# Optimization experiments

Measured on AMD Instinct MI355X. Metric: run time of the kernel, lower is better.

The kernel has to match this reference:

```python
import jax, jax.numpy as jnp
import numpy as np

B, T, C = 16, 2048, 1024
HEAD = 64

def setup_inputs() -> dict:
    key = jax.random.key(0)
    kx, kq, kk, kv = jax.random.split(key, 4)
    x = jax.random.normal(kx, (B, T, C), dtype=jnp.float32)
    s = 1.0 / np.sqrt(C)
    Wq = jax.random.normal(kq, (C, HEAD), dtype=jnp.float32) * s
    Wk = jax.random.normal(kk, (C, HEAD), dtype=jnp.float32) * s
    Wv = jax.random.normal(kv, (C, HEAD), dtype=jnp.float32) * s
    return {"x": x, "Wq": Wq, "Wk": Wk, "Wv": Wv}

def reference(x, Wq, Wk, Wv):
    Bb, Tt, Cc = x.shape
    q = jnp.einsum('btc,ch->bth', x, Wq)  # [B,T,H]
    k = jnp.einsum('btc,ch->bth', x, Wk)
    v = jnp.einsum('btc,ch->bth', x, Wv)
    # NOTE: source scales by C**-0.5 (n_embd), not head_size**-0.5
    scores = jnp.einsum('bth,bsh->bts', q, k) * (Cc ** -0.5)  # [B,T,T]
    causal = jnp.tril(jnp.ones((Tt, Tt), dtype=bool))
    scores = jnp.where(causal, scores, -jnp.inf)
    attn = jax.nn.softmax(scores, axis=-1)  # dropout p=0 -> identity
    out = jnp.einsum('bts,bsh->bth', attn, v)  # [B,T,H]
    return out
```

## Files before the change

### kernel.cpp

```cpp
#include <hip/hip_runtime.h>

typedef __bf16 bf16;
typedef __bf16 bf16x2 __attribute__((ext_vector_type(2)));
typedef __bf16 bf16x4 __attribute__((ext_vector_type(4)));
typedef __bf16 bf16x8 __attribute__((ext_vector_type(8)));
typedef float f32x4 __attribute__((ext_vector_type(4)));

#define TT_ 2048
#define CC_ 1024
#define HH_ 64

#define SCALE2 0.045084221f

static __device__ __forceinline__ unsigned pack_bf16(float a, float b) {
    union { bf16x2 h; unsigned u; } z;
    z.h = bf16x2{(bf16)a, (bf16)b};
    return z.u;
}
static __device__ __forceinline__ void plswap32(unsigned &a, unsigned &b) {
    asm("v_permlane32_swap_b32 %0, %1" : "+v"(a), "+v"(b));
}
static __device__ __forceinline__ void plswap16(unsigned &a, unsigned &b) {
    asm("v_permlane16_swap_b32 %0, %1" : "+v"(a), "+v"(b));
}

__global__ __launch_bounds__(256) void prep_w(const float* __restrict__ Wq,
                                              const float* __restrict__ Wk,
                                              const float* __restrict__ Wv,
                                              bf16* __restrict__ Wt) {
    __shared__ bf16 Ls[64 * 65];
    const int m  = blockIdx.x >> 4;
    const int k0 = (blockIdx.x & 15) * 64;
    const float* W = (m == 0) ? Wq : (m == 1) ? Wk : Wv;
    const int tid = threadIdx.x;
    #pragma unroll
    for (int j = 0; j < 4; ++j) {
        int idx = tid + 256 * j;
        int r   = idx >> 4;
        int c4  = (idx & 15) * 4;
        float4 w = *(const float4*)&W[(size_t)(k0 + r) * HH_ + c4];
        Ls[r * 65 + c4 + 0] = (bf16)w.x;
        Ls[r * 65 + c4 + 1] = (bf16)w.y;
        Ls[r * 65 + c4 + 2] = (bf16)w.z;
        Ls[r * 65 + c4 + 3] = (bf16)w.w;
    }
    __syncthreads();
    #pragma unroll
    for (int j = 0; j < 4; ++j) {
        int idx = tid + 256 * j;
        int n   = idx >> 4;
        int kc  = (idx & 15) * 4;
        bf16x4 v;
        #pragma unroll
        for (int i = 0; i < 4; ++i) v[i] = Ls[(kc + i) * 65 + n];
        *(bf16x4*)&Wt[m * 65536 + n * 1024 + k0 + kc] = v;
    }
}

__global__ __launch_bounds__(256, 3) void qkv_kernel(const float* __restrict__ x,
                                                     const bf16* __restrict__ Wt,
                                                     bf16* __restrict__ qb,
                                                     bf16* __restrict__ kb,
                                                     bf16* __restrict__ vt) {
    __shared__ __align__(16) bf16 Xs[64 * 72];
    const int tid  = threadIdx.x;
    const int wave = tid >> 6;
    const int lane = tid & 15;
    const int quad = (tid & 63) >> 4;
    const int m0   = blockIdx.x * 64;

    f32x4 acc[4][3];
    #pragma unroll
    for (int i = 0; i < 4; ++i)
        #pragma unroll
        for (int j = 0; j < 3; ++j) acc[i][j] = f32x4{0.f, 0.f, 0.f, 0.f};

    const float* xrow[4];
    #pragma unroll
    for (int rt = 0; rt < 4; ++rt)
        xrow[rt] = x + (size_t)(m0 + rt * 16 + lane) * CC_ + quad * 8;
    const bf16* wbase = Wt + (size_t)(wave * 48 + lane) * 1024 + quad * 8;

    for (int kbi = 0; kbi < 16; ++kbi) {
        const int k0 = kbi * 64;
        bf16x8 afr[2][4];
        #pragma unroll
        for (int step = 0; step < 2; ++step)
            #pragma unroll
            for (int rt = 0; rt < 4; ++rt) {
                float4 a = *(const float4*)&xrow[rt][k0 + step * 32];
                float4 b = *(const float4*)&xrow[rt][k0 + step * 32 + 4];
                afr[step][rt] = bf16x8{(bf16)a.x, (bf16)a.y, (bf16)a.z, (bf16)a.w,
                                       (bf16)b.x, (bf16)b.y, (bf16)b.z, (bf16)b.w};
            }
        bf16x8 bfr[2][3];
        #pragma unroll
        for (int step = 0; step < 2; ++step)
            #pragma unroll
            for (int ct = 0; ct < 3; ++ct)
                bfr[step][ct] = *(const bf16x8*)&wbase[(size_t)(ct * 16) * 1024 + k0 + step * 32];
        #pragma unroll
        for (int step = 0; step < 2; ++step)
            #pragma unroll
            for (int ct = 0; ct < 3; ++ct)
                #pragma unroll
                for (int rt = 0; rt < 4; ++rt)
                    acc[rt][ct] = __builtin_amdgcn_mfma_f32_16x16x32_bf16(afr[step][rt], bfr[step][ct], acc[rt][ct], 0, 0, 0);
    }

    const int bb = m0 >> 11;
    const int t0 = m0 & 2047;
    #pragma unroll
    for (int ct = 0; ct < 3; ++ct) {
        int c0 = wave * 48 + ct * 16;
        if (c0 < 64) {
            int h = c0 + lane;
            #pragma unroll
            for (int rt = 0; rt < 4; ++rt)
                #pragma unroll
                for (int r = 0; r < 4; ++r)
                    qb[(size_t)(m0 + rt * 16 + quad * 4 + r) * HH_ + h] = (bf16)(acc[rt][ct][r] * SCALE2);
        } else if (c0 < 128) {
            int h = (c0 - 64) + lane;
            #pragma unroll
            for (int rt = 0; rt < 4; ++rt)
                #pragma unroll
                for (int r = 0; r < 4; ++r)
                    kb[(size_t)(m0 + rt * 16 + quad * 4 + r) * HH_ + h] = (bf16)acc[rt][ct][r];
        } else {
            int h = (c0 - 128) + lane;
            #pragma unroll
            for (int rt = 0; rt < 4; ++rt)
                #pragma unroll
                for (int r = 0; r < 4; ++r)
                    Xs[(rt * 16 + quad * 4 + r) * 72 + h] = (bf16)acc[rt][ct][r];
        }
    }
    __syncthreads();
    {
        int h  = tid >> 2;
        int tc = (tid & 3) * 16;
        bf16x8 v0, v1;
        #pragma unroll
        for (int i = 0; i < 8; ++i) v0[i] = Xs[(tc + i) * 72 + h];
        #pragma unroll
        for (int i = 0; i < 8; ++i) v1[i] = Xs[(tc + 8 + i) * 72 + h];
        bf16* dst = &vt[(size_t)bb * HH_ * TT_ + (size_t)h * TT_ + t0 + tc];
        *(bf16x8*)dst = v0;
        *(bf16x8*)(dst + 8) = v1;
    }
}

__global__ __launch_bounds__(256, 2) void attn_kernel(const bf16* __restrict__ qb,
                                                      const bf16* __restrict__ kb,
                                                      const bf16* __restrict__ vt,
                                                      float* __restrict__ out) {
    __shared__ __align__(16) bf16 Ks[128 * 72];
    __shared__ __align__(16) bf16 Vs[64 * 136];

    const int tid  = threadIdx.x;
    const int wave = tid >> 6;
    const int lane = tid & 15;
    const int quad = (tid & 63) >> 4;

    const int j  = blockIdx.x;
    const int bb = j & 15;
    const int p  = j >> 4;
    const int qi = (p < 16) ? p : 47 - p;
    const int nch = (qi >> 1) + 1;

    const int qrow  = qi * 64 + wave * 16;
    const int qg    = qrow + lane;
    const int qmaxw = qrow + 15;

    const int krow = tid >> 3, kc8 = (tid & 7) * 8;
    const int vh   = tid >> 4, vc8 = (tid & 15) * 8;
    const bf16* kp = kb + (size_t)(bb * TT_ + krow) * HH_ + kc8;
    const bf16* vp = vt + (size_t)bb * HH_ * TT_ + (size_t)vh * TT_ + vc8;

    bf16x8 kr[4], vvr[4];
    #pragma unroll
    for (int j2 = 0; j2 < 4; ++j2) kr[j2]  = *(const bf16x8*)&kp[(size_t)j2 * 32 * HH_];
    #pragma unroll
    for (int j2 = 0; j2 < 4; ++j2) vvr[j2] = *(const bf16x8*)&vp[j2 * 16 * TT_];

    bf16x8 aq[2];
    #pragma unroll
    for (int step = 0; step < 2; ++step)
        aq[step] = *(const bf16x8*)&qb[(size_t)(bb * TT_ + qg) * HH_ + step * 32 + quad * 8];

    bf16x8 vones;
    #pragma unroll
    for (int i = 0; i < 8; ++i) vones[i] = (bf16)1.0f;

    f32x4 o_acc[4];
    #pragma unroll
    for (int ht = 0; ht < 4; ++ht) o_acc[ht] = f32x4{0.f, 0.f, 0.f, 0.f};
    f32x4 lacc = f32x4{0.f, 0.f, 0.f, 0.f};

    for (int c = 0; c < nch; ++c) {
        const int s0 = c * 128;
        __syncthreads();
        #pragma unroll
        for (int j2 = 0; j2 < 4; ++j2) *(bf16x8*)&Ks[(krow + 32 * j2) * 72 + kc8] = kr[j2];
        #pragma unroll
        for (int j2 = 0; j2 < 4; ++j2) *(bf16x8*)&Vs[(vh + 16 * j2) * 136 + vc8]  = vvr[j2];
        __syncthreads();
        if (c + 1 < nch) {
            #pragma unroll
            for (int j2 = 0; j2 < 4; ++j2)
                kr[j2] = *(const bf16x8*)&kp[(size_t)((c + 1) * 128 + j2 * 32) * HH_];
            #pragma unroll
            for (int j2 = 0; j2 < 4; ++j2)
                vvr[j2] = *(const bf16x8*)&vp[(c + 1) * 128 + j2 * 16 * TT_];
        }

        const bool msk = (c == nch - 1);
        #pragma unroll
        for (int w = 0; w < 4; ++w) {
            if (msk && (s0 + w * 32 > qmaxw)) continue;
            const bool haveB = !msk || (s0 + w * 32 + 16 <= qmaxw);

            f32x4 sA = {0.f, 0.f, 0.f, 0.f};
            f32x4 sB = {0.f, 0.f, 0.f, 0.f};
            __builtin_amdgcn_s_setprio(1);
            {
                bf16x8 ak0 = *(const bf16x8*)&Ks[(w * 32 + lane) * 72 + quad * 8];
                bf16x8 ak1 = *(const bf16x8*)&Ks[(w * 32 + lane) * 72 + 32 + quad * 8];
                sA = __builtin_amdgcn_mfma_f32_16x16x32_bf16(ak0, aq[0], sA, 0, 0, 0);
                sA = __builtin_amdgcn_mfma_f32_16x16x32_bf16(ak1, aq[1], sA, 0, 0, 0);
            }
            if (haveB) {
                bf16x8 bk0 = *(const bf16x8*)&Ks[(w * 32 + 16 + lane) * 72 + quad * 8];
                bf16x8 bk1 = *(const bf16x8*)&Ks[(w * 32 + 16 + lane) * 72 + 32 + quad * 8];
                sB = __builtin_amdgcn_mfma_f32_16x16x32_bf16(bk0, aq[0], sB, 0, 0, 0);
                sB = __builtin_amdgcn_mfma_f32_16x16x32_bf16(bk1, aq[1], sB, 0, 0, 0);
            }
            __builtin_amdgcn_s_setprio(0);

            const int kA0 = s0 + w * 32 + quad * 4;
            float eA[4], eB[4];
            #pragma unroll
            for (int r = 0; r < 4; ++r) {
                float e = __builtin_amdgcn_exp2f(sA[r]);
                if (msk && (kA0 + r > qg)) e = 0.f;
                eA[r] = e;
            }
            if (haveB) {
                #pragma unroll
                for (int r = 0; r < 4; ++r) {
                    float e = __builtin_amdgcn_exp2f(sB[r]);
                    if (msk && (kA0 + 16 + r > qg)) e = 0.f;
                    eB[r] = e;
                }
            } else {
                #pragma unroll
                for (int r = 0; r < 4; ++r) eB[r] = 0.f;
            }

            unsigned d0 = pack_bf16(eA[0], eA[1]);
            unsigned d1 = pack_bf16(eA[2], eA[3]);
            unsigned d2 = pack_bf16(eB[0], eB[1]);
            unsigned d3 = pack_bf16(eB[2], eB[3]);
            plswap32(d0, d2);
            plswap16(d0, d2);
            plswap32(d1, d3);
            plswap16(d1, d3);
            union { unsigned u[4]; bf16x8 v; } apu;
            apu.u[0] = d0; apu.u[1] = d1; apu.u[2] = d2; apu.u[3] = d3;

            __builtin_amdgcn_s_setprio(1);
            #pragma unroll
            for (int ht = 0; ht < 4; ++ht) {
                bf16x8 bv = *(const bf16x8*)&Vs[(ht * 16 + lane) * 136 + w * 32 + quad * 8];
                o_acc[ht] = __builtin_amdgcn_mfma_f32_16x16x32_bf16(apu.v, bv, o_acc[ht], 0, 0, 0);
            }
            lacc = __builtin_amdgcn_mfma_f32_16x16x32_bf16(apu.v, vones, lacc, 0, 0, 0);
            __builtin_amdgcn_s_setprio(0);
        }
    }

    float inv[4];
    #pragma unroll
    for (int r = 0; r < 4; ++r) inv[r] = __builtin_amdgcn_rcpf(lacc[r]);
    #pragma unroll
    for (int ht = 0; ht < 4; ++ht)
        #pragma unroll
        for (int r = 0; r < 4; ++r)
            out[(size_t)(bb * TT_ + qrow + quad * 4 + r) * HH_ + ht * 16 + lane] = o_acc[ht][r] * inv[r];
}

extern "C" void kernel_launch(void* const* d_in, const int* in_sizes, int n_in,
                              void* d_out, int out_size, void* d_ws, size_t ws_size,
                              hipStream_t stream) {
    const float* x  = (const float*)d_in[0];
    const float* Wq = (const float*)d_in[1];
    const float* Wk = (const float*)d_in[2];
    const float* Wv = (const float*)d_in[3];
    float* out = (float*)d_out;

    char* ws = (char*)d_ws;
    bf16*  qb = (bf16*)(ws);
    bf16*  kb = (bf16*)(ws + 4194304);
    bf16*  vt = (bf16*)(ws + 8388608);
    bf16*  Wt = (bf16*)(ws + 12582912);

    prep_w<<<48, 256, 0, stream>>>(Wq, Wk, Wv, Wt);
    qkv_kernel<<<512, 256, 0, stream>>>(x, Wt, qb, kb, vt);
    attn_kernel<<<512, 256, 0, stream>>>(qb, kb, vt, out);
}
```

Before: 289.2 us.

## Prefetch x tiles into per-wave LDS double buffer and halve QKV tile rows

New measurement: 293.1 us. Within noise of the previous version (+1.4%).

```diff
diff --git a/kernel.cpp b/kernel.cpp
--- a/kernel.cpp
+++ b/kernel.cpp
@@ -57,42 +57,53 @@
     }
 }
 
-__global__ __launch_bounds__(256, 3) void qkv_kernel(const float* __restrict__ x,
+__global__ __launch_bounds__(256, 4) void qkv_kernel(const float* __restrict__ x,
                                                      const bf16* __restrict__ Wt,
                                                      bf16* __restrict__ qb,
                                                      bf16* __restrict__ kb,
                                                      bf16* __restrict__ vt) {
-    __shared__ __align__(16) bf16 Xs[64 * 72];
+    __shared__ __align__(16) bf16 Xs[4][2][32 * 72];
     const int tid  = threadIdx.x;
     const int wave = tid >> 6;
+    const int wl   = tid & 63;
     const int lane = tid & 15;
     const int quad = (tid & 63) >> 4;
-    const int m0   = blockIdx.x * 64;
-
-    f32x4 acc[4][3];
-    #pragma unroll
-    for (int i = 0; i < 4; ++i)
+    const int m0   = blockIdx.x * 32;
+
+    bf16 (*myXs)[32 * 72] = Xs[wave];
+
+    const int srow = wl >> 1;
+    const int scol = (wl & 1) * 32;
+    const float* xsrc = x + (size_t)(m0 + srow) * CC_ + scol;
+    const bf16*  wbase = Wt + (size_t)(wave * 48 + lane) * 1024 + quad * 8;
+
+    f32x4 acc[2][3];
+    #pragma unroll
+    for (int i = 0; i < 2; ++i)
         #pragma unroll
         for (int j = 0; j < 3; ++j) acc[i][j] = f32x4{0.f, 0.f, 0.f, 0.f};
 
-    const float* xrow[4];
-    #pragma unroll
-    for (int rt = 0; rt < 4; ++rt)
-        xrow[rt] = x + (size_t)(m0 + rt * 16 + lane) * CC_ + quad * 8;
-    const bf16* wbase = Wt + (size_t)(wave * 48 + lane) * 1024 + quad * 8;
+    float4 pf[8];
+    #pragma unroll
+    for (int i = 0; i < 8; ++i) pf[i] = *(const float4*)&xsrc[i * 4];
+    #pragma unroll
+    for (int i = 0; i < 4; ++i) {
+        bf16x8 bv = {(bf16)pf[2*i].x, (bf16)pf[2*i].y, (bf16)pf[2*i].z, (bf16)pf[2*i].w,
+                     (bf16)pf[2*i+1].x, (bf16)pf[2*i+1].y, (bf16)pf[2*i+1].z, (bf16)pf[2*i+1].w};
+        *(bf16x8*)&myXs[0][srow * 72 + scol + i * 8] = bv;
+    }
+    #pragma unroll
+    for (int i = 0; i < 8; ++i) pf[i] = *(const float4*)&xsrc[64 + i * 4];
 
     for (int kbi = 0; kbi < 16; ++kbi) {
-        const int k0 = kbi * 64;
-        bf16x8 afr[2][4];
+        const int cur = kbi & 1;
+        const int k0  = kbi * 64;
+        bf16x8 afr[2][2];
         #pragma unroll
         for (int step = 0; step < 2; ++step)
             #pragma unroll
-            for (int rt = 0; rt < 4; ++rt) {
-                float4 a = *(const float4*)&xrow[rt][k0 + step * 32];
-                float4 b = *(const float4*)&xrow[rt][k0 + step * 32 + 4];
-                afr[step][rt] = bf16x8{(bf16)a.x, (bf16)a.y, (bf16)a.z, (bf16)a.w,
-                                       (bf16)b.x, (bf16)b.y, (bf16)b.z, (bf16)b.w};
-            }
+            for (int rt = 0; rt < 2; ++rt)
+                afr[step][rt] = *(const bf16x8*)&myXs[cur][(rt * 16 + lane) * 72 + step * 32 + quad * 8];
         bf16x8 bfr[2][3];
         #pragma unroll
         for (int step = 0; step < 2; ++step)
@@ -104,50 +115,60 @@
             #pragma unroll
             for (int ct = 0; ct < 3; ++ct)
                 #pragma unroll
-                for (int rt = 0; rt < 4; ++rt)
+                for (int rt = 0; rt < 2; ++rt)
                     acc[rt][ct] = __builtin_amdgcn_mfma_f32_16x16x32_bf16(afr[step][rt], bfr[step][ct], acc[rt][ct], 0, 0, 0);
+        if (kbi < 15) {
+            #pragma unroll
+            for (int i = 0; i < 4; ++i) {
+                bf16x8 bv = {(bf16)pf[2*i].x, (bf16)pf[2*i].y, (bf16)pf[2*i].z, (bf16)pf[2*i].w,
+                             (bf16)pf[2*i+1].x, (bf16)pf[2*i+1].y, (bf16)pf[2*i+1].z, (bf16)pf[2*i+1].w};
+                *(bf16x8*)&myXs[cur ^ 1][srow * 72 + scol + i * 8] = bv;
+            }
+        }
+        if (kbi < 14) {
+            #pragma unroll
+            for (int i = 0; i < 8; ++i)
+                pf[i] = *(const float4*)&xsrc[(kbi + 2) * 64 + i * 4];
+        }
     }
 
     const int bb = m0 >> 11;
     const int t0 = m0 & 2047;
+    __syncthreads();
     #pragma unroll
     for (int ct = 0; ct < 3; ++ct) {
         int c0 = wave * 48 + ct * 16;
         if (c0 < 64) {
             int h = c0 + lane;
             #pragma unroll
-            for (int rt = 0; rt < 4; ++rt)
+            for (int rt = 0; rt < 2; ++rt)
                 #pragma unroll
                 for (int r = 0; r < 4; ++r)
                     qb[(size_t)(m0 + rt * 16 + quad * 4 + r) * HH_ + h] = (bf16)(acc[rt][ct][r] * SCALE2);
         } else if (c0 < 128) {
             int h = (c0 - 64) + lane;
             #pragma unroll
-            for (int rt = 0; rt < 4; ++rt)
+            for (int rt = 0; rt < 2; ++rt)
                 #pragma unroll
                 for (int r = 0; r < 4; ++r)
                     kb[(size_t)(m0 + rt * 16 + quad * 4 + r) * HH_ + h] = (bf16)acc[rt][ct][r];
         } else {
             int h = (c0 - 128) + lane;
             #pragma unroll
-            for (int rt = 0; rt < 4; ++rt)
+            for (int rt = 0; rt < 2; ++rt)
                 #pragma unroll
                 for (int r = 0; r < 4; ++r)
-                    Xs[(rt * 16 + quad * 4 + r) * 72 + h] = (bf16)acc[rt][ct][r];
+                    Xs[0][0][(rt * 16 + quad * 4 + r) * 72 + h] = (bf16)acc[rt][ct][r];
         }
     }
     __syncthreads();
     {
         int h  = tid >> 2;
-        int tc = (tid & 3) * 16;
-        bf16x8 v0, v1;
-        #pragma unroll
-        for (int i = 0; i < 8; ++i) v0[i] = Xs[(tc + i) * 72 + h];
-        #pragma unroll
-        for (int i = 0; i < 8; ++i) v1[i] = Xs[(tc + 8 + i) * 72 + h];
-        bf16* dst = &vt[(size_t)bb * HH_ * TT_ + (size_t)h * TT_ + t0 + tc];
-        *(bf16x8*)dst = v0;
-        *(bf16x8*)(dst + 8) = v1;
+        int tc = (tid & 3) * 8;
+        bf16x8 v0;
+        #pragma unroll
+        for (int i = 0; i < 8; ++i) v0[i] = Xs[0][0][(tc + i) * 72 + h];
+        *(bf16x8*)&vt[(size_t)bb * HH_ * TT_ + (size_t)h * TT_ + t0 + tc] = v0;
     }
 }
 
@@ -306,6 +327,6 @@
     bf16*  Wt = (bf16*)(ws + 12582912);
 
     prep_w<<<48, 256, 0, stream>>>(Wq, Wk, Wv, Wt);
-    qkv_kernel<<<512, 256, 0, stream>>>(x, Wt, qb, kb, vt);
+    qkv_kernel<<<1024, 256, 0, stream>>>(x, Wt, qb, kb, vt);
     attn_kernel<<<512, 256, 0, stream>>>(qb, kb, vt, out);
 }
```
